# Kernel tuning notes

Hardware: AMD Instinct MI355X
Metric: run time of the kernel (lower is better)

Reference implementation:

```python
import jax, jax.numpy as jnp
import numpy as np

TNEI = 2
TOPK = 4
NEIGH = 2 * TNEI + 1  # window size = 5


def _normalize(x, eps=1e-12):
    # matches torch F.normalize(dim=-1)
    n = jnp.linalg.norm(x, axis=-1, keepdims=True)
    return x / jnp.maximum(n, eps)


def setup_inputs() -> dict:
    key = jax.random.key(0)
    ks = jax.random.split(key, 10)
    B, T, C = 32, 256, 128
    x = jax.random.normal(ks[0], (B, T, C), jnp.float32)
    radj = jax.random.randint(ks[1], (B, T, T), 0, 2).astype(jnp.int32)
    inxs = jax.random.randint(ks[2], (B, T, TOPK), 0, T)
    s = 1.0 / np.sqrt(C)
    W_pf = jax.random.normal(ks[3], (C, C), jnp.float32) * s
    W_ns = jax.random.normal(ks[4], (C, C), jnp.float32) * s
    W_v = jax.random.normal(ks[5], (C, C), jnp.float32) * s
    v_pf = jax.random.normal(ks[6], (NEIGH,), jnp.float32)
    g_pf = jnp.linalg.norm(v_pf)[None]  # weight_norm gain, shape (1,)
    v_ns = jax.random.normal(ks[7], (TOPK,), jnp.float32)
    g_ns = jnp.linalg.norm(v_ns)[None]
    return dict(x=x, radj=radj, inxs=inxs, W_pf=W_pf, W_ns=W_ns, W_v=W_v,
                v_pf=v_pf, g_pf=g_pf, v_ns=v_ns, g_ns=g_ns)


def reference(x, radj, inxs, W_pf, W_ns, W_v, v_pf, g_pf, v_ns, g_ns):
    B, T, C = x.shape
    pf = _normalize(x @ W_pf.T)
    ns = _normalize(x @ W_ns.T)
    v = x @ W_v.T
    # windowed neighbor indices, identical to _tneigh_mask(mode='all')
    i = jnp.arange(T)
    start = jnp.clip(i - TNEI, 0, T - NEIGH)
    nbr = start[:, None] + jnp.arange(NEIGH)[None, :]  # (T, NEIGH)
    ctx = pf[:, nbr]  # (B, T, NEIGH, C) — replaces one-hot ctxinx einsum
    # pairwise window similarity: (B,T,T,n,n)
    sim = jnp.einsum('bxic,byjc->bxyij', ctx, ctx)
    # AdaptiveMaxPool2d((n,1)) == max over the last (key-window) axis
    sim_pf = sim.max(axis=-1)  # (B,T,T,n)
    w_pf = g_pf[0] * v_pf / jnp.linalg.norm(v_pf)  # weight-norm agg_pf
    sim_pf = jnp.einsum('bxyi,i->bxy', sim_pf, w_pf)
    # topk-neighbor branch: inxs gathers ns rows (replaces one-hot einsum)
    ns_q = ns[jnp.arange(B)[:, None, None], inxs]  # (B,T,TOPK,C)
    sim_ns = jnp.einsum('bxnc,byc->bxyn', ns_q, ns)  # (B,T,T,TOPK)
    w_ns = g_ns[0] * v_ns / jnp.linalg.norm(v_ns)  # weight-norm agg_ns
    sim_ns = jnp.einsum('bxyn,n->bxy', sim_ns, w_ns)
    # adjacency mask: 0 -> -1e22, >0 -> 0
    mask = jnp.where(radj == 0, jnp.float32(-1e22), jnp.float32(0.0))
    attn = jax.nn.softmax(sim_pf + sim_ns + mask, axis=-1)  # (B,T,T)
    return jnp.einsum('bkt,btd->bkd', attn, v)  # (B,T,C)
```

## Files before the change

### kernel.cpp

```cpp
#include <hip/hip_runtime.h>
#include <hip/hip_bf16.h>
#include <math.h>


#define TT 256
#define CC 128

__global__ __launch_bounds__(256) void proj_kernel(
    const float* __restrict__ x,
    const float* __restrict__ W0, const float* __restrict__ W1, const float* __restrict__ W2,
    float* __restrict__ o0, float* __restrict__ o1, float* __restrict__ o2)
{
    __shared__ float xs[32][36];
    __shared__ float Ws[128][36];
    const int tid = threadIdx.x, ty = tid >> 4, tx = tid & 15;
    const int row0 = blockIdx.x * 32;
    const int m = blockIdx.y;
    const float* __restrict__ W = (m == 0) ? W0 : (m == 1) ? W1 : W2;
    float* __restrict__ o = (m == 0) ? o0 : (m == 1) ? o1 : o2;
    float acc[2][8] = {};

    for (int k0 = 0; k0 < CC; k0 += 32) {
        __syncthreads();
        {
            int r = tid >> 3, q = (tid & 7) * 4;
            *(float4*)&xs[r][q] = *(const float4*)&x[(row0 + r) * CC + k0 + q];
        }
        for (int i = 0; i < 4; i++) {
            int flat = i * 256 + tid, r = flat >> 3, q = (flat & 7) * 4;
            *(float4*)&Ws[r][q] = *(const float4*)&W[r * CC + k0 + q];
        }
        __syncthreads();
        for (int kq = 0; kq < 32; kq += 4) {
            float4 av[2], bv[8];
            for (int u = 0; u < 2; u++) av[u] = *(float4*)&xs[ty + 16 * u][kq];
            for (int w = 0; w < 8; w++) bv[w] = *(float4*)&Ws[tx + 16 * w][kq];
            for (int u = 0; u < 2; u++)
                for (int w = 0; w < 8; w++) {
                    acc[u][w] = fmaf(av[u].x, bv[w].x, acc[u][w]);
                    acc[u][w] = fmaf(av[u].y, bv[w].y, acc[u][w]);
                    acc[u][w] = fmaf(av[u].z, bv[w].z, acc[u][w]);
                    acc[u][w] = fmaf(av[u].w, bv[w].w, acc[u][w]);
                }
        }
    }
    for (int u = 0; u < 2; u++) {
        float inv = 1.f;
        if (m < 2) {
            float ss = 0.f;
            for (int w = 0; w < 8; w++) ss += acc[u][w] * acc[u][w];
            for (int off = 8; off; off >>= 1) ss += __shfl_xor(ss, off);
            inv = 1.f / fmaxf(sqrtf(ss), 1e-12f);
        }
        int row = row0 + ty + 16 * u;
        for (int w = 0; w < 8; w++)
            o[row * CC + tx + 16 * w] = acc[u][w] * inv;
    }
}

__global__ __launch_bounds__(256, 4) void gram_combined(
    const float* __restrict__ pf, const float* __restrict__ ns,
    const int* __restrict__ inxs, const float* __restrict__ v_ns,
    const float* __restrict__ g_ns, float* __restrict__ G, float* __restrict__ S)
{
    __shared__ float As[64][36], Bs[64][36];
    const int tid = threadIdx.x, ty = tid >> 4, tx = tid & 15;
    const int m0 = blockIdx.x * 64, n0 = blockIdx.y * 64;
    const int b = blockIdx.z >> 1, half = blockIdx.z & 1;
    const float* __restrict__ Pb = pf + b * TT * CC;
    const float* __restrict__ Nb = ns + b * TT * CC;

    float w0 = 0.f, w1 = 0.f, w2 = 0.f, w3 = 0.f;
    int4 id0 = {0, 0, 0, 0}, id1 = {0, 0, 0, 0};
    if (half) {
        float n2 = v_ns[0]*v_ns[0] + v_ns[1]*v_ns[1] + v_ns[2]*v_ns[2] + v_ns[3]*v_ns[3];
        float sc = g_ns[0] / sqrtf(n2);
        w0 = sc*v_ns[0]; w1 = sc*v_ns[1]; w2 = sc*v_ns[2]; w3 = sc*v_ns[3];
        id0 = *(const int4*)&inxs[(b * TT + m0 + (tid >> 3)) * 4];
        id1 = *(const int4*)&inxs[(b * TT + m0 + 32 + (tid >> 3)) * 4];
    }

    float acc[4][4] = {};
    for (int k0 = 0; k0 < CC; k0 += 32) {
        __syncthreads();
        if (!half) {
            for (int i = 0; i < 2; i++) {
                int flat = i * 256 + tid, r = flat >> 3, q = (flat & 7) * 4;
                *(float4*)&As[r][q] = *(const float4*)&Pb[(m0 + r) * CC + k0 + q];
                *(float4*)&Bs[r][q] = *(const float4*)&Pb[(n0 + r) * CC + k0 + q];
            }
        } else {
            for (int i = 0; i < 2; i++) {
                int flat = i * 256 + tid, r = flat >> 3, q = (flat & 7) * 4;
                int4 id = i ? id1 : id0;
                float4 aa = *(const float4*)&Nb[id.x * CC + k0 + q];
                float4 ab = *(const float4*)&Nb[id.y * CC + k0 + q];
                float4 ac = *(const float4*)&Nb[id.z * CC + k0 + q];
                float4 ad = *(const float4*)&Nb[id.w * CC + k0 + q];
                float4 r4;
                r4.x = w0*aa.x + w1*ab.x + w2*ac.x + w3*ad.x;
                r4.y = w0*aa.y + w1*ab.y + w2*ac.y + w3*ad.y;
                r4.z = w0*aa.z + w1*ab.z + w2*ac.z + w3*ad.z;
                r4.w = w0*aa.w + w1*ab.w + w2*ac.w + w3*ad.w;
                *(float4*)&As[r][q] = r4;
                *(float4*)&Bs[r][q] = *(const float4*)&Nb[(n0 + r) * CC + k0 + q];
            }
        }
        __syncthreads();
        for (int kq = 0; kq < 32; kq += 4) {
            float4 av[4], bv[4];
            for (int u = 0; u < 4; u++) av[u] = *(float4*)&As[ty + 16 * u][kq];
            for (int w = 0; w < 4; w++) bv[w] = *(float4*)&Bs[tx + 16 * w][kq];
            for (int u = 0; u < 4; u++)
                for (int w = 0; w < 4; w++) {
                    acc[u][w] = fmaf(av[u].x, bv[w].x, acc[u][w]);
                    acc[u][w] = fmaf(av[u].y, bv[w].y, acc[u][w]);
                    acc[u][w] = fmaf(av[u].z, bv[w].z, acc[u][w]);
                    acc[u][w] = fmaf(av[u].w, bv[w].w, acc[u][w]);
                }
        }
    }
    float* __restrict__ Cb = (half ? S : G) + b * TT * TT;
    for (int u = 0; u < 4; u++)
        for (int w = 0; w < 4; w++)
            Cb[(m0 + ty + 16 * u) * TT + n0 + tx + 16 * w] = acc[u][w];
}

__global__ __launch_bounds__(256, 4) void logits_softmax_pv(
    const float* __restrict__ G, const float* __restrict__ S,
    const int* __restrict__ radj, const float* __restrict__ v_pf,
    const float* __restrict__ g_pf, const float* __restrict__ V,
    float* __restrict__ out)
{
    __shared__ float Gs[20 * 256];
    __shared__ float attn[16 * 260];
    __shared__ float redm[16][4];
    __shared__ float reds[16][4];
    const int tid = threadIdx.x;
    const int xt = blockIdx.x, b = blockIdx.y;
    const int x0 = xt * 16;
    const int rbase = min(max(x0 - 2, 0), TT - 5);
    for (int i = 0; i < 5; i++) {
        int flat = i * 256 + tid, ri = flat >> 6, q = (flat & 63) * 4;
        int r = min(rbase + ri, TT - 1);
        *(float4*)&Gs[ri * 256 + q] = *(const float4*)&G[b * TT * TT + r * TT + q];
    }
    float n2 = 0.f;
    for (int i = 0; i < 5; i++) n2 += v_pf[i] * v_pf[i];
    float sc = g_pf[0] / sqrtf(n2);
    float wpf[5];
    for (int i = 0; i < 5; i++) wpf[i] = sc * v_pf[i];
    __syncthreads();

    const int y = tid;
    const int sy = min(max(y - 2, 0), TT - 5);
    float lv[16];
    for (int xi = 0; xi < 16; xi++) {
        int gx = x0 + xi;
        int sx = min(max(gx - 2, 0), TT - 5);
        float s = 0.f;
        for (int i = 0; i < 5; i++) {
            const float* row = Gs + (sx - rbase + i) * 256 + sy;
            float mx = row[0];
            for (int j = 1; j < 5; j++) mx = fmaxf(mx, row[j]);
            s = fmaf(wpf[i], mx, s);
        }
        s += S[b * TT * TT + gx * TT + y];
        if (radj[(b * TT + gx) * TT + y] == 0) s += -1e22f;
        lv[xi] = s;
    }
    const int lane = tid & 63, wv = tid >> 6;
    for (int xi = 0; xi < 16; xi++) {
        float v = lv[xi];
        for (int o = 32; o; o >>= 1) v = fmaxf(v, __shfl_xor(v, o));
        if (lane == 0) redm[xi][wv] = v;
    }
    __syncthreads();
    for (int xi = 0; xi < 16; xi++) {
        float mx = fmaxf(fmaxf(redm[xi][0], redm[xi][1]), fmaxf(redm[xi][2], redm[xi][3]));
        float e = __expf(lv[xi] - mx);
        attn[xi * 260 + y] = e;
        for (int o = 32; o; o >>= 1) e += __shfl_xor(e, o);
        if (lane == 0) reds[xi][wv] = e;
    }
    float* Vs = Gs;
    const int r = tid >> 4, tx = tid & 15;
    const float* __restrict__ Vb = V + b * TT * CC;
    float4 acc0 = {0, 0, 0, 0}, acc1 = {0, 0, 0, 0};
    for (int k0 = 0; k0 < TT; k0 += 32) {
        __syncthreads();
        for (int i = 0; i < 4; i++) {
            int flat = i * 256 + tid, kk = flat >> 5, q = (flat & 31) * 4;
            *(float4*)&Vs[kk * 132 + q] = *(const float4*)&Vb[(k0 + kk) * CC + q];
        }
        __syncthreads();
        for (int kk = 0; kk < 32; kk++) {
            float a = attn[r * 260 + k0 + kk];
            float4 b0 = *(float4*)&Vs[kk * 132 + 4 * tx];
            float4 b1 = *(float4*)&Vs[kk * 132 + 64 + 4 * tx];
            acc0.x = fmaf(a, b0.x, acc0.x); acc0.y = fmaf(a, b0.y, acc0.y);
            acc0.z = fmaf(a, b0.z, acc0.z); acc0.w = fmaf(a, b0.w, acc0.w);
            acc1.x = fmaf(a, b1.x, acc1.x); acc1.y = fmaf(a, b1.y, acc1.y);
            acc1.z = fmaf(a, b1.z, acc1.z); acc1.w = fmaf(a, b1.w, acc1.w);
        }
    }
    float sm = reds[r][0] + reds[r][1] + reds[r][2] + reds[r][3];
    float rinv = 1.f / sm;
    acc0.x *= rinv; acc0.y *= rinv; acc0.z *= rinv; acc0.w *= rinv;
    acc1.x *= rinv; acc1.y *= rinv; acc1.z *= rinv; acc1.w *= rinv;
    int m = x0 + r;
    *(float4*)&out[b * TT * CC + m * CC + 4 * tx]      = acc0;
    *(float4*)&out[b * TT * CC + m * CC + 64 + 4 * tx] = acc1;
}

extern "C" void kernel_launch(void* const* d_in, const int* in_sizes, int n_in,
                              void* d_out, int out_size, void* d_ws, size_t ws_size,
                              hipStream_t stream) {
    const float* x    = (const float*)d_in[0];
    const int*   radj = (const int*)d_in[1];
    const int*   inxs = (const int*)d_in[2];
    const float* Wpf  = (const float*)d_in[3];
    const float* Wns  = (const float*)d_in[4];
    const float* Wv   = (const float*)d_in[5];
    const float* v_pf = (const float*)d_in[6];
    const float* g_pf = (const float*)d_in[7];
    const float* v_ns = (const float*)d_in[8];
    const float* g_ns = (const float*)d_in[9];
    float* out = (float*)d_out;

    float* ws = (float*)d_ws;
    float* pf = ws;
    float* ns = ws + (1u << 20);
    float* vv = ws + 2u * (1u << 20);
    float* G  = ws + 4u * (1u << 20);
    float* S  = ws + 6u * (1u << 20);

    proj_kernel<<<dim3(256, 3), 256, 0, stream>>>(x, Wpf, Wns, Wv, pf, ns, vv);
    gram_combined<<<dim3(4, 4, 64), 256, 0, stream>>>(pf, ns, inxs, v_ns, g_ns, G, S);
    logits_softmax_pv<<<dim3(16, 32), 256, 0, stream>>>(G, S, radj, v_pf, g_pf, vv, out);
}
```

Measured before the change: 149.5 us.

## Use split-bf16 MFMA for Gram, precompute row maxima, retile projection and PV

```diff
diff --git a/kernel.cpp b/kernel.cpp
--- a/kernel.cpp
+++ b/kernel.cpp
@@ -1,29 +1,41 @@
 #include <hip/hip_runtime.h>
-#include <hip/hip_bf16.h>
 #include <math.h>
 
 
 #define TT 256
 #define CC 128
+
+using bf16x8 = __attribute__((ext_vector_type(8))) short;
+using f32x4  = __attribute__((ext_vector_type(4))) float;
+
+__device__ __forceinline__ short bf_hi(float x) {
+    unsigned u = __float_as_uint(x);
+    return (short)((u + 0x7FFFu + ((u >> 16) & 1u)) >> 16);
+}
+__device__ __forceinline__ void bf_split(float x, short& h, short& l) {
+    h = bf_hi(x);
+    float hf = __uint_as_float(((unsigned)(unsigned short)h) << 16);
+    l = bf_hi(x - hf);
+}
 
 __global__ __launch_bounds__(256) void proj_kernel(
     const float* __restrict__ x,
     const float* __restrict__ W0, const float* __restrict__ W1, const float* __restrict__ W2,
     float* __restrict__ o0, float* __restrict__ o1, float* __restrict__ o2)
 {
-    __shared__ float xs[32][36];
+    __shared__ float xs[64][36];
     __shared__ float Ws[128][36];
     const int tid = threadIdx.x, ty = tid >> 4, tx = tid & 15;
-    const int row0 = blockIdx.x * 32;
+    const int row0 = blockIdx.x * 64;
     const int m = blockIdx.y;
     const float* __restrict__ W = (m == 0) ? W0 : (m == 1) ? W1 : W2;
     float* __restrict__ o = (m == 0) ? o0 : (m == 1) ? o1 : o2;
-    float acc[2][8] = {};
+    float acc[4][8] = {};
 
     for (int k0 = 0; k0 < CC; k0 += 32) {
         __syncthreads();
-        {
-            int r = tid >> 3, q = (tid & 7) * 4;
+        for (int i = 0; i < 2; i++) {
+            int flat = i * 256 + tid, r = flat >> 3, q = (flat & 7) * 4;
             *(float4*)&xs[r][q] = *(const float4*)&x[(row0 + r) * CC + k0 + q];
         }
         for (int i = 0; i < 4; i++) {
@@ -32,10 +44,10 @@
         }
         __syncthreads();
         for (int kq = 0; kq < 32; kq += 4) {
-            float4 av[2], bv[8];
-            for (int u = 0; u < 2; u++) av[u] = *(float4*)&xs[ty + 16 * u][kq];
+            float4 av[4], bv[8];
+            for (int u = 0; u < 4; u++) av[u] = *(float4*)&xs[ty + 16 * u][kq];
             for (int w = 0; w < 8; w++) bv[w] = *(float4*)&Ws[tx + 16 * w][kq];
-            for (int u = 0; u < 2; u++)
+            for (int u = 0; u < 4; u++)
                 for (int w = 0; w < 8; w++) {
                     acc[u][w] = fmaf(av[u].x, bv[w].x, acc[u][w]);
                     acc[u][w] = fmaf(av[u].y, bv[w].y, acc[u][w]);
@@ -44,7 +56,7 @@
                 }
         }
     }
-    for (int u = 0; u < 2; u++) {
+    for (int u = 0; u < 4; u++) {
         float inv = 1.f;
         if (m < 2) {
             float ss = 0.f;
@@ -58,17 +70,18 @@
     }
 }
 
-__global__ __launch_bounds__(256, 4) void gram_combined(
+__global__ __launch_bounds__(256, 4) void gram_mfma(
     const float* __restrict__ pf, const float* __restrict__ ns,
     const int* __restrict__ inxs, const float* __restrict__ v_ns,
     const float* __restrict__ g_ns, float* __restrict__ G, float* __restrict__ S)
 {
-    __shared__ float As[64][36], Bs[64][36];
-    const int tid = threadIdx.x, ty = tid >> 4, tx = tid & 15;
+    __shared__ short Ah[64 * 40], Al[64 * 40], Bh[64 * 40], Bl[64 * 40];
+    const int tid = threadIdx.x;
     const int m0 = blockIdx.x * 64, n0 = blockIdx.y * 64;
     const int b = blockIdx.z >> 1, half = blockIdx.z & 1;
     const float* __restrict__ Pb = pf + b * TT * CC;
     const float* __restrict__ Nb = ns + b * TT * CC;
+    const float* __restrict__ Bsrc = half ? Nb : Pb;
 
     float w0 = 0.f, w1 = 0.f, w2 = 0.f, w3 = 0.f;
     int4 id0 = {0, 0, 0, 0}, id1 = {0, 0, 0, 0};
@@ -80,62 +93,81 @@
         id1 = *(const int4*)&inxs[(b * TT + m0 + 32 + (tid >> 3)) * 4];
     }
 
-    float acc[4][4] = {};
+    const int lane = tid & 63, wave = tid >> 6;
+    const int wm = wave >> 1, wn = wave & 1;
+    const int quad = lane >> 4, lr = lane & 15;
+    f32x4 z4 = {0.f, 0.f, 0.f, 0.f};
+    f32x4 acc[2][2] = {{z4, z4}, {z4, z4}};
+
     for (int k0 = 0; k0 < CC; k0 += 32) {
         __syncthreads();
-        if (!half) {
-            for (int i = 0; i < 2; i++) {
-                int flat = i * 256 + tid, r = flat >> 3, q = (flat & 7) * 4;
-                *(float4*)&As[r][q] = *(const float4*)&Pb[(m0 + r) * CC + k0 + q];
-                *(float4*)&Bs[r][q] = *(const float4*)&Pb[(n0 + r) * CC + k0 + q];
-            }
-        } else {
-            for (int i = 0; i < 2; i++) {
-                int flat = i * 256 + tid, r = flat >> 3, q = (flat & 7) * 4;
+        for (int i = 0; i < 2; i++) {
+            int flat = i * 256 + tid, r = flat >> 3, q = (flat & 7) * 4;
+            float4 a4;
+            if (!half) {
+                a4 = *(const float4*)&Pb[(m0 + r) * CC + k0 + q];
+            } else {
                 int4 id = i ? id1 : id0;
                 float4 aa = *(const float4*)&Nb[id.x * CC + k0 + q];
                 float4 ab = *(const float4*)&Nb[id.y * CC + k0 + q];
                 float4 ac = *(const float4*)&Nb[id.z * CC + k0 + q];
                 float4 ad = *(const float4*)&Nb[id.w * CC + k0 + q];
-                float4 r4;
-                r4.x = w0*aa.x + w1*ab.x + w2*ac.x + w3*ad.x;
-                r4.y = w0*aa.y + w1*ab.y + w2*ac.y + w3*ad.y;
-                r4.z = w0*aa.z + w1*ab.z + w2*ac.z + w3*ad.z;
-                r4.w = w0*aa.w + w1*ab.w + w2*ac.w + w3*ad.w;
-                *(float4*)&As[r][q] = r4;
-                *(float4*)&Bs[r][q] = *(const float4*)&Nb[(n0 + r) * CC + k0 + q];
-            }
-        }
-        __syncthreads();
-        for (int kq = 0; kq < 32; kq += 4) {
-            float4 av[4], bv[4];
-            for (int u = 0; u < 4; u++) av[u] = *(float4*)&As[ty + 16 * u][kq];
-            for (int w = 0; w < 4; w++) bv[w] = *(float4*)&Bs[tx + 16 * w][kq];
-            for (int u = 0; u < 4; u++)
-                for (int w = 0; w < 4; w++) {
-                    acc[u][w] = fmaf(av[u].x, bv[w].x, acc[u][w]);
-                    acc[u][w] = fmaf(av[u].y, bv[w].y, acc[u][w]);
-                    acc[u][w] = fmaf(av[u].z, bv[w].z, acc[u][w]);
-                    acc[u][w] = fmaf(av[u].w, bv[w].w, acc[u][w]);
-                }
+                a4.x = w0*aa.x + w1*ab.x + w2*ac.x + w3*ad.x;
+                a4.y = w0*aa.y + w1*ab.y + w2*ac.y + w3*ad.y;
+                a4.z = w0*aa.z + w1*ab.z + w2*ac.z + w3*ad.z;
+                a4.w = w0*aa.w + w1*ab.w + w2*ac.w + w3*ad.w;
+            }
+            float4 b4 = *(const float4*)&Bsrc[(n0 + r) * CC + k0 + q];
+            short4 h4, l4;
+            bf_split(a4.x, h4.x, l4.x); bf_split(a4.y, h4.y, l4.y);
+            bf_split(a4.z, h4.z, l4.z); bf_split(a4.w, h4.w, l4.w);
+            *(short4*)&Ah[r * 40 + q] = h4; *(short4*)&Al[r * 40 + q] = l4;
+            bf_split(b4.x, h4.x, l4.x); bf_split(b4.y, h4.y, l4.y);
+            bf_split(b4.z, h4.z, l4.z); bf_split(b4.w, h4.w, l4.w);
+            *(short4*)&Bh[r * 40 + q] = h4; *(short4*)&Bl[r * 40 + q] = l4;
+        }
+        __syncthreads();
+        bf16x8 bh[2], bl[2];
+        for (int tn = 0; tn < 2; tn++) {
+            int br = (32 * wn + 16 * tn + lr) * 40 + quad * 8;
+            bh[tn] = *(bf16x8*)&Bh[br];
+            bl[tn] = *(bf16x8*)&Bl[br];
+        }
+        for (int tm = 0; tm < 2; tm++) {
+            int ar = (32 * wm + 16 * tm + lr) * 40 + quad * 8;
+            bf16x8 ah = *(bf16x8*)&Ah[ar];
+            bf16x8 al = *(bf16x8*)&Al[ar];
+            for (int tn = 0; tn < 2; tn++) {
+                acc[tm][tn] = __builtin_amdgcn_mfma_f32_16x16x32_bf16(ah, bh[tn], acc[tm][tn], 0, 0, 0);
+                acc[tm][tn] = __builtin_amdgcn_mfma_f32_16x16x32_bf16(ah, bl[tn], acc[tm][tn], 0, 0, 0);
+                acc[tm][tn] = __builtin_amdgcn_mfma_f32_16x16x32_bf16(al, bh[tn], acc[tm][tn], 0, 0, 0);
+            }
         }
     }
     float* __restrict__ Cb = (half ? S : G) + b * TT * TT;
-    for (int u = 0; u < 4; u++)
-        for (int w = 0; w < 4; w++)
-            Cb[(m0 + ty + 16 * u) * TT + n0 + tx + 16 * w] = acc[u][w];
-}
-
-__global__ __launch_bounds__(256, 4) void logits_softmax_pv(
+    for (int tm = 0; tm < 2; tm++)
+        for (int tn = 0; tn < 2; tn++) {
+            int rb = m0 + 32 * wm + 16 * tm + quad * 4;
+            int cb = n0 + 32 * wn + 16 * tn + lr;
+            for (int reg = 0; reg < 4; reg++)
+                Cb[(rb + reg) * TT + cb] = acc[tm][tn][reg];
+        }
+}
+
+#define GS_ 0
+#define RM_ 5120
+#define AT_ 10320
+#define RD_ 14480
+#define RMX_ 14544
+#define VS_ 0
+#define PP_ 4224
+__global__ __launch_bounds__(256, 2) void fused_smax_pv(
     const float* __restrict__ G, const float* __restrict__ S,
     const int* __restrict__ radj, const float* __restrict__ v_pf,
     const float* __restrict__ g_pf, const float* __restrict__ V,
     float* __restrict__ out)
 {
-    __shared__ float Gs[20 * 256];
-    __shared__ float attn[16 * 260];
-    __shared__ float redm[16][4];
-    __shared__ float reds[16][4];
+    __shared__ float lds[14608];
     const int tid = threadIdx.x;
     const int xt = blockIdx.x, b = blockIdx.y;
     const int x0 = xt * 16;
@@ -143,7 +175,7 @@
     for (int i = 0; i < 5; i++) {
         int flat = i * 256 + tid, ri = flat >> 6, q = (flat & 63) * 4;
         int r = min(rbase + ri, TT - 1);
-        *(float4*)&Gs[ri * 256 + q] = *(const float4*)&G[b * TT * TT + r * TT + q];
+        *(float4*)&lds[GS_ + ri * 256 + q] = *(const float4*)&G[b * TT * TT + r * TT + q];
     }
     float n2 = 0.f;
     for (int i = 0; i < 5; i++) n2 += v_pf[i] * v_pf[i];
@@ -154,63 +186,88 @@
 
     const int y = tid;
     const int sy = min(max(y - 2, 0), TT - 5);
+    for (int i = 0; i < 20; i++) {
+        const float* row = &lds[GS_ + i * 256 + sy];
+        float mx = row[0];
+        for (int j = 1; j < 5; j++) mx = fmaxf(mx, row[j]);
+        lds[RM_ + i * 260 + y] = mx;
+    }
     float lv[16];
     for (int xi = 0; xi < 16; xi++) {
-        int gx = x0 + xi;
-        int sx = min(max(gx - 2, 0), TT - 5);
+        int sxr = min(max(x0 + xi - 2, 0), TT - 5) - rbase;
         float s = 0.f;
-        for (int i = 0; i < 5; i++) {
-            const float* row = Gs + (sx - rbase + i) * 256 + sy;
-            float mx = row[0];
-            for (int j = 1; j < 5; j++) mx = fmaxf(mx, row[j]);
-            s = fmaf(wpf[i], mx, s);
-        }
-        s += S[b * TT * TT + gx * TT + y];
-        if (radj[(b * TT + gx) * TT + y] == 0) s += -1e22f;
+        for (int i = 0; i < 5; i++)
+            s = fmaf(wpf[i], lds[RM_ + (sxr + i) * 260 + y], s);
+        s += S[b * TT * TT + (x0 + xi) * TT + y];
+        if (radj[(b * TT + x0 + xi) * TT + y] == 0) s += -1e22f;
         lv[xi] = s;
     }
     const int lane = tid & 63, wv = tid >> 6;
     for (int xi = 0; xi < 16; xi++) {
         float v = lv[xi];
         for (int o = 32; o; o >>= 1) v = fmaxf(v, __shfl_xor(v, o));
-        if (lane == 0) redm[xi][wv] = v;
+        if (lane == 0) lds[RMX_ + xi * 4 + wv] = v;
     }
     __syncthreads();
     for (int xi = 0; xi < 16; xi++) {
-        float mx = fmaxf(fmaxf(redm[xi][0], redm[xi][1]), fmaxf(redm[xi][2], redm[xi][3]));
+        float mx = fmaxf(fmaxf(lds[RMX_ + xi * 4], lds[RMX_ + xi * 4 + 1]),
+                         fmaxf(lds[RMX_ + xi * 4 + 2], lds[RMX_ + xi * 4 + 3]));
         float e = __expf(lv[xi] - mx);
-        attn[xi * 260 + y] = e;
+        lds[AT_ + xi * 260 + y] = e;
         for (int o = 32; o; o >>= 1) e += __shfl_xor(e, o);
-        if (lane == 0) reds[xi][wv] = e;
-    }
-    float* Vs = Gs;
-    const int r = tid >> 4, tx = tid & 15;
+        if (lane == 0) lds[RD_ + xi * 4 + wv] = e;
+    }
+    const int tx = tid & 15, qt = (tid >> 4) & 3, w = tid >> 6;
     const float* __restrict__ Vb = V + b * TT * CC;
-    float4 acc0 = {0, 0, 0, 0}, acc1 = {0, 0, 0, 0};
-    for (int k0 = 0; k0 < TT; k0 += 32) {
+    float4 a0[4] = {}, a1[4] = {};
+    for (int c = 0; c < 8; c++) {
+        int kk0 = c * 32;
         __syncthreads();
         for (int i = 0; i < 4; i++) {
             int flat = i * 256 + tid, kk = flat >> 5, q = (flat & 31) * 4;
-            *(float4*)&Vs[kk * 132 + q] = *(const float4*)&Vb[(k0 + kk) * CC + q];
-        }
-        __syncthreads();
-        for (int kk = 0; kk < 32; kk++) {
-            float a = attn[r * 260 + k0 + kk];
-            float4 b0 = *(float4*)&Vs[kk * 132 + 4 * tx];
-            float4 b1 = *(float4*)&Vs[kk * 132 + 64 + 4 * tx];
-            acc0.x = fmaf(a, b0.x, acc0.x); acc0.y = fmaf(a, b0.y, acc0.y);
-            acc0.z = fmaf(a, b0.z, acc0.z); acc0.w = fmaf(a, b0.w, acc0.w);
-            acc1.x = fmaf(a, b1.x, acc1.x); acc1.y = fmaf(a, b1.y, acc1.y);
-            acc1.z = fmaf(a, b1.z, acc1.z); acc1.w = fmaf(a, b1.w, acc1.w);
-        }
-    }
-    float sm = reds[r][0] + reds[r][1] + reds[r][2] + reds[r][3];
+            *(float4*)&lds[VS_ + kk * 132 + q] = *(const float4*)&Vb[(kk0 + kk) * CC + q];
+        }
+        __syncthreads();
+        for (int s = 0; s < 2; s++) {
+            int kl = w * 8 + s * 4;
+            float atv[4][4];
+            for (int j = 0; j < 4; j++) {
+                float4 t = *(float4*)&lds[AT_ + (qt * 4 + j) * 260 + kk0 + kl];
+                atv[j][0] = t.x; atv[j][1] = t.y; atv[j][2] = t.z; atv[j][3] = t.w;
+            }
+            for (int kk = 0; kk < 4; kk++) {
+                float4 v0 = *(float4*)&lds[VS_ + (kl + kk) * 132 + 8 * tx];
+                float4 v1 = *(float4*)&lds[VS_ + (kl + kk) * 132 + 8 * tx + 4];
+                for (int j = 0; j < 4; j++) {
+                    float a = atv[j][kk];
+                    a0[j].x = fmaf(a, v0.x, a0[j].x); a0[j].y = fmaf(a, v0.y, a0[j].y);
+                    a0[j].z = fmaf(a, v0.z, a0[j].z); a0[j].w = fmaf(a, v0.w, a0[j].w);
+                    a1[j].x = fmaf(a, v1.x, a1[j].x); a1[j].y = fmaf(a, v1.y, a1[j].y);
+                    a1[j].z = fmaf(a, v1.z, a1[j].z); a1[j].w = fmaf(a, v1.w, a1[j].w);
+                }
+            }
+        }
+    }
+    __syncthreads();
+    for (int j = 0; j < 4; j++) {
+        *(float4*)&lds[PP_ + (w * 16 + qt * 4 + j) * 128 + 8 * tx]     = a0[j];
+        *(float4*)&lds[PP_ + (w * 16 + qt * 4 + j) * 128 + 8 * tx + 4] = a1[j];
+    }
+    __syncthreads();
+    const int q = tid >> 4, c0 = (tid & 15) * 8;
+    float4 r0 = {0, 0, 0, 0}, r1 = {0, 0, 0, 0};
+    for (int ww = 0; ww < 4; ww++) {
+        float4 p0 = *(float4*)&lds[PP_ + (ww * 16 + q) * 128 + c0];
+        float4 p1 = *(float4*)&lds[PP_ + (ww * 16 + q) * 128 + c0 + 4];
+        r0.x += p0.x; r0.y += p0.y; r0.z += p0.z; r0.w += p0.w;
+        r1.x += p1.x; r1.y += p1.y; r1.z += p1.z; r1.w += p1.w;
+    }
+    float sm = lds[RD_ + q * 4] + lds[RD_ + q * 4 + 1] + lds[RD_ + q * 4 + 2] + lds[RD_ + q * 4 + 3];
     float rinv = 1.f / sm;
-    acc0.x *= rinv; acc0.y *= rinv; acc0.z *= rinv; acc0.w *= rinv;
-    acc1.x *= rinv; acc1.y *= rinv; acc1.z *= rinv; acc1.w *= rinv;
-    int m = x0 + r;
-    *(float4*)&out[b * TT * CC + m * CC + 4 * tx]      = acc0;
-    *(float4*)&out[b * TT * CC + m * CC + 64 + 4 * tx] = acc1;
+    r0.x *= rinv; r0.y *= rinv; r0.z *= rinv; r0.w *= rinv;
+    r1.x *= rinv; r1.y *= rinv; r1.z *= rinv; r1.w *= rinv;
+    *(float4*)&out[b * TT * CC + (x0 + q) * CC + c0]     = r0;
+    *(float4*)&out[b * TT * CC + (x0 + q) * CC + c0 + 4] = r1;
 }
 
 extern "C" void kernel_launch(void* const* d_in, const int* in_sizes, int n_in,
@@ -235,7 +292,7 @@
     float* G  = ws + 4u * (1u << 20);
     float* S  = ws + 6u * (1u << 20);
 
-    proj_kernel<<<dim3(256, 3), 256, 0, stream>>>(x, Wpf, Wns, Wv, pf, ns, vv);
-    gram_combined<<<dim3(4, 4, 64), 256, 0, stream>>>(pf, ns, inxs, v_ns, g_ns, G, S);
-    logits_softmax_pv<<<dim3(16, 32), 256, 0, stream>>>(G, S, radj, v_pf, g_pf, vv, out);
-}
+    proj_kernel<<<dim3(128, 3), 256, 0, stream>>>(x, Wpf, Wns, Wv, pf, ns, vv);
+    gram_mfma<<<dim3(4, 4, 64), 256, 0, stream>>>(pf, ns, inxs, v_ns, g_ns, G, S);
+    fused_smax_pv<<<dim3(16, 32), 256, 0, stream>>>(G, S, radj, v_pf, g_pf, vv, out);
+}
```

Measured after the change: 129.8 us. 13.2% less time.
